# Kernel optimization log

Hardware: AMD Instinct MI355X
Metric: run time of the kernel (lower is better)

## Reference

```python
import jax, jax.numpy as jnp
import numpy as np

L = 2          # lstm_layers
H = 512        # state_size
E = 512        # embedding_size
V = 512        # latent_vocab_size
T = 100        # max_dec_len
START = V - 1  # start_id
B = 128        # batch
M = 256        # mem_len
NS = 4         # num_sample


def setup_inputs() -> dict:
    key = jax.random.key(0)
    ks = jax.random.split(key, 12)
    s = 0.05
    return {
        "y": jax.random.normal(ks[0], (B, H), jnp.float32),
        "kv_emb": jax.random.normal(ks[1], (B, M, H), jnp.float32),
        "kv_mask": jnp.ones((B, M), dtype=bool),
        "z_mask": jnp.ones((B, T), jnp.float32),
        "emb": jax.random.normal(ks[2], (V, E), jnp.float32) * s,
        "W_h0": jax.random.normal(ks[3], (L * H, H), jnp.float32) * s,
        "b_h0": jnp.zeros((L * H,), jnp.float32),
        "W_c0": jax.random.normal(ks[4], (L * H, H), jnp.float32) * s,
        "b_c0": jnp.zeros((L * H,), jnp.float32),
        "W_ih": jax.random.normal(ks[5], (L, 4 * H, E), jnp.float32) * s,
        "W_hh": jax.random.normal(ks[6], (L, 4 * H, H), jnp.float32) * s,
        "b_ih": jnp.zeros((L, 4 * H), jnp.float32),
        "b_hh": jnp.zeros((L, 4 * H), jnp.float32),
        "W_attn": jax.random.normal(ks[7], (H, H), jnp.float32) * s,
        "W_cproj": jax.random.normal(ks[8], (H, 2 * H), jnp.float32) * s,
        "b_cproj": jnp.zeros((H,), jnp.float32),
        "W_out": jax.random.normal(ks[9], (V, H), jnp.float32) * s,
        "b_out": jnp.zeros((V,), jnp.float32),
        "num_sample": NS,
    }


def reference(y, kv_emb, kv_mask, z_mask, emb, W_h0, b_h0, W_c0, b_c0,
              W_ih, W_hh, b_ih, b_hh, W_attn, W_cproj, b_cproj, W_out, b_out,
              num_sample):
    n = int(num_sample)
    Bn = B * n
    # view(B,1,..).repeat(1,n,..).view(B*n,..)  ==  repeat along axis 0 (sample-minor)
    y_r = jnp.repeat(y, n, axis=0)                      # [Bn, H]
    kv_r = jnp.repeat(kv_emb, n, axis=0)                # [Bn, M, H]
    mask_add = jnp.where(jnp.repeat(kv_mask, n, axis=0), 0.0, -1e9).astype(jnp.float32)

    # init_state: project y -> per-layer h, c
    h = (y_r @ W_h0.T + b_h0).reshape(Bn, L, H).transpose(1, 0, 2)  # [L, Bn, H]
    c = (y_r @ W_c0.T + b_c0).reshape(Bn, L, H).transpose(1, 0, 2)
    x0 = emb[jnp.full((Bn,), START)]                    # start-token embedding
    base_key = jax.random.key(42)

    def step(carry, t):
        h, c, x = carry
        hs, cs = [], []
        for l in range(L):  # stacked LSTM cells (PyTorch gate order i,f,g,o)
            g = x @ W_ih[l].T + b_ih[l] + h[l] @ W_hh[l].T + b_hh[l]
            i_, f_, g_, o_ = jnp.split(g, 4, axis=-1)
            cn = jax.nn.sigmoid(f_) * c[l] + jax.nn.sigmoid(i_) * jnp.tanh(g_)
            hn = jax.nn.sigmoid(o_) * jnp.tanh(cn)
            hs.append(hn); cs.append(cn); x = hn
        out = x                                         # top-layer h, [Bn, H]
        # bilinear attention over kv memory with mask
        scores = jnp.einsum('bd,bmd->bm', out @ W_attn.T, kv_r) + mask_add
        attn = jax.nn.softmax(scores, axis=-1)
        ctx = jnp.einsum('bm,bmd->bd', attn, kv_r)
        out2 = jnp.concatenate([out, ctx], axis=-1) @ W_cproj.T + b_cproj
        logits = out2 @ W_out.T + b_out                 # output_proj
        logp = jax.nn.log_softmax(logits, axis=-1)
        # Categorical sample (strategy='unconstrained')
        idx = jax.random.categorical(jax.random.fold_in(base_key, t), logits)
        slp = jnp.take_along_axis(logp, idx[:, None], axis=-1)[:, 0]
        ent = (-jnp.exp(logp) * logp).sum(-1).mean()
        return (jnp.stack(hs), jnp.stack(cs), emb[idx]), (idx, slp, ent)

    _, (ids, slps, ents) = jax.lax.scan(step, (h, c, x0), jnp.arange(T))
    z_ids = ids.T.reshape(B, n, T)                      # [B, n, T] int
    z_states = emb[z_ids]                               # [B, n, T, E]
    stepwise = slps.T.reshape(B, n, T)
    z_lp = (stepwise * z_mask[:, None, :]).sum(-1)      # [B, n]
    ent_z = ents.mean()
    return z_ids, z_states, z_lp, stepwise, ent_z
```

## Files before the change

### kernel.cpp

```cpp
#include <hip/hip_runtime.h>
#include <hip/hip_bf16.h>

#define BATCH 128
#define NSAMP 4
#define BN    512
#define HID   512
#define EMBD  512
#define VOC   512
#define TLEN  100
#define MLEN  256
#define NGATE 2048

#define NPART 8

#define O_ZID     0L
#define O_ZSTATES 51200L
#define O_ZLP     26265600L
#define O_STEP    26266112L
#define O_ENT     26317312L
#define O_TOTAL   26317313L

#define OFF_H    0L
#define OFF_C    524288L
#define OFF_X    1048576L
#define OFF_G    1310720L
#define OFF_Q    9699328L
#define OFF_CTX  11796480L
#define OFF_O2   12058624L
#define OFF_LG   14155776L
#define OFF_YR   16252928L
#define OFF_BG   16515072L
#define OFF_ENT  16519168L
#define OFF_SLP  16519296L
#define WS_FLOATS 16570496L

#define GPSTRIDE 1048576L
#define SPSTRIDE 262144L

__device__ float g_ws[WS_FLOATS];
__device__ int   g_ids[TLEN * BN];

__device__ __forceinline__ unsigned rotl32(unsigned x, int r) {
  return (x << r) | (x >> (32 - r));
}
__device__ __forceinline__ void threefry2x32(unsigned k0, unsigned k1,
                                             unsigned& x0, unsigned& x1) {
  unsigned k2 = k0 ^ k1 ^ 0x1BD11BDAu;
#define TF_R(r) { x0 += x1; x1 = rotl32(x1, r); x1 ^= x0; }
  x0 += k0; x1 += k1;
  TF_R(13) TF_R(15) TF_R(26) TF_R(6)
  x0 += k1; x1 += k2 + 1u;
  TF_R(17) TF_R(29) TF_R(16) TF_R(24)
  x0 += k2; x1 += k0 + 2u;
  TF_R(13) TF_R(15) TF_R(26) TF_R(6)
  x0 += k0; x1 += k1 + 3u;
  TF_R(17) TF_R(29) TF_R(16) TF_R(24)
  x0 += k1; x1 += k2 + 4u;
  TF_R(13) TF_R(15) TF_R(26) TF_R(6)
  x0 += k2; x1 += k0 + 5u;
#undef TF_R
}

__device__ __forceinline__ float gumbel_from_bits(unsigned bits) {
  unsigned fb = (bits >> 9) | 0x3F800000u;
  float f = __uint_as_float(fb) - 1.0f;
  const float TINY = 1.17549435e-38f;
  float u = fmaxf(f + TINY, TINY);
  return -logf(-logf(u));
}

__device__ __forceinline__ float sigf(float x) {
  return 0.5f + 0.5f * tanhf(0.5f * x);
}

__device__ __forceinline__ float4 add4(float4 a, float4 b) {
  a.x += b.x; a.y += b.y; a.z += b.z; a.w += b.w; return a;
}

__global__ __launch_bounds__(64) void gemmsk(
    long offA1, int lda1, int P1, long strideP1,
    const float* __restrict__ B1, int ldb1, int K1,
    long offA2, int lda2,
    const float* __restrict__ B2, int ldb2,
    const float* __restrict__ biasExt, long biasOff,
    long offC, int ldc, int Kc)
{
  __shared__ float As[16][64];
  __shared__ float Bs[16][64];
  const int t  = threadIdx.x;
  const int tm = t >> 3;
  const int tn = t & 7;
  const int m0 = blockIdx.y * 64;
  const int n0 = blockIdx.x * 64;
  const int kp = blockIdx.z;

  int kbase = kp * Kc;
  const float* A; const float* B; int lda, ldb, P; long strideP;
  if (kbase < K1) {
    A = g_ws + offA1; B = B1; lda = lda1; ldb = ldb1; P = P1; strideP = strideP1;
  } else {
    A = g_ws + offA2; B = B2; lda = lda2; ldb = ldb2; P = 1; strideP = 0;
    kbase -= K1;
  }

  float acc[8][8];
#pragma unroll
  for (int i = 0; i < 8; ++i)
#pragma unroll
    for (int j = 0; j < 8; ++j) acc[i][j] = 0.f;

  for (int k0 = 0; k0 < Kc; k0 += 16) {
    const int kg = kbase + k0;
    const float* pa = A + (size_t)(m0 + t) * lda + kg;
    float4 a0, a1, a2, a3;
    {
      const float4* q4 = (const float4*)pa;
      a0 = q4[0]; a1 = q4[1]; a2 = q4[2]; a3 = q4[3];
      for (int p = 1; p < P; ++p) {
        const float4* r4 = (const float4*)(pa + (size_t)p * strideP);
        a0 = add4(a0, r4[0]); a1 = add4(a1, r4[1]);
        a2 = add4(a2, r4[2]); a3 = add4(a3, r4[3]);
      }
    }
    const float4* pb = (const float4*)(B + (size_t)(n0 + t) * ldb + kg);
    float4 b0 = pb[0], b1 = pb[1], b2 = pb[2], b3 = pb[3];

    __syncthreads();
    As[ 0][t] = a0.x; As[ 1][t] = a0.y; As[ 2][t] = a0.z; As[ 3][t] = a0.w;
    As[ 4][t] = a1.x; As[ 5][t] = a1.y; As[ 6][t] = a1.z; As[ 7][t] = a1.w;
    As[ 8][t] = a2.x; As[ 9][t] = a2.y; As[10][t] = a2.z; As[11][t] = a2.w;
    As[12][t] = a3.x; As[13][t] = a3.y; As[14][t] = a3.z; As[15][t] = a3.w;
    Bs[ 0][t] = b0.x; Bs[ 1][t] = b0.y; Bs[ 2][t] = b0.z; Bs[ 3][t] = b0.w;
    Bs[ 4][t] = b1.x; Bs[ 5][t] = b1.y; Bs[ 6][t] = b1.z; Bs[ 7][t] = b1.w;
    Bs[ 8][t] = b2.x; Bs[ 9][t] = b2.y; Bs[10][t] = b2.z; Bs[11][t] = b2.w;
    Bs[12][t] = b3.x; Bs[13][t] = b3.y; Bs[14][t] = b3.z; Bs[15][t] = b3.w;
    __syncthreads();

#pragma unroll
    for (int k = 0; k < 16; ++k) {
      float av[8], bv[8];
      *(float4*)&av[0] = *(const float4*)&As[k][tm * 8];
      *(float4*)&av[4] = *(const float4*)&As[k][tm * 8 + 4];
      *(float4*)&bv[0] = *(const float4*)&Bs[k][tn * 8];
      *(float4*)&bv[4] = *(const float4*)&Bs[k][tn * 8 + 4];
#pragma unroll
      for (int i = 0; i < 8; ++i)
#pragma unroll
        for (int j = 0; j < 8; ++j)
          acc[i][j] += av[i] * bv[j];
    }
  }

  const int Mtot = gridDim.y * 64;
  float* C = g_ws + offC + (size_t)kp * (size_t)Mtot * ldc;
  const float* bias = nullptr;
  if (kp == 0)
    bias = biasExt ? biasExt : (biasOff >= 0 ? g_ws + biasOff : nullptr);
#pragma unroll
  for (int i = 0; i < 8; ++i) {
    const int row = m0 + tm * 8 + i;
    const int col = n0 + tn * 8;
    float4 o0, o1;
    o0.x = acc[i][0]; o0.y = acc[i][1]; o0.z = acc[i][2]; o0.w = acc[i][3];
    o1.x = acc[i][4]; o1.y = acc[i][5]; o1.z = acc[i][6]; o1.w = acc[i][7];
    if (bias) {
      o0.x += bias[col];     o0.y += bias[col + 1];
      o0.z += bias[col + 2]; o0.w += bias[col + 3];
      o1.x += bias[col + 4]; o1.y += bias[col + 5];
      o1.z += bias[col + 6]; o1.w += bias[col + 7];
    }
    *(float4*)(C + (size_t)row * ldc + col)     = o0;
    *(float4*)(C + (size_t)row * ldc + col + 4) = o1;
  }
}

__global__ __launch_bounds__(256) void gemm2(
    long offA1, int lda1,
    const float* __restrict__ B1, int ldb1, int K1,
    long offA2, int lda2,
    const float* __restrict__ B2, int ldb2, int K2,
    const float* __restrict__ biasExt, long biasOff,
    long offC, int ldc)
{
  __shared__ float As[16][68];
  __shared__ float Bs[16][68];
  const int tid = threadIdx.x;
  const int tx  = tid & 15;
  const int ty  = tid >> 4;
  const int ldr = tid >> 2;
  const int ldk = (tid & 3) << 2;
  const int m0 = blockIdx.y * 64;
  const int n0 = blockIdx.x * 64;
  float acc[4][4] = {{0.f}};

  for (int seg = 0; seg < 2; ++seg) {
    const float* A = g_ws + (seg ? offA2 : offA1);
    const float* B = seg ? B2 : B1;
    const int lda = seg ? lda2 : lda1;
    const int ldb = seg ? ldb2 : ldb1;
    const int K   = seg ? K2  : K1;
    for (int k0 = 0; k0 < K; k0 += 16) {
      float4 av = *(const float4*)(A + (size_t)(m0 + ldr) * lda + k0 + ldk);
      float4 bv = *(const float4*)(B + (size_t)(n0 + ldr) * ldb + k0 + ldk);
      __syncthreads();
      As[ldk + 0][ldr] = av.x; As[ldk + 1][ldr] = av.y;
      As[ldk + 2][ldr] = av.z; As[ldk + 3][ldr] = av.w;
      Bs[ldk + 0][ldr] = bv.x; Bs[ldk + 1][ldr] = bv.y;
      Bs[ldk + 2][ldr] = bv.z; Bs[ldk + 3][ldr] = bv.w;
      __syncthreads();
#pragma unroll
      for (int k = 0; k < 16; ++k) {
        float4 a = *(const float4*)&As[k][ty * 4];
        float4 b = *(const float4*)&Bs[k][tx * 4];
        acc[0][0] += a.x * b.x; acc[0][1] += a.x * b.y; acc[0][2] += a.x * b.z; acc[0][3] += a.x * b.w;
        acc[1][0] += a.y * b.x; acc[1][1] += a.y * b.y; acc[1][2] += a.y * b.z; acc[1][3] += a.y * b.w;
        acc[2][0] += a.z * b.x; acc[2][1] += a.z * b.y; acc[2][2] += a.z * b.z; acc[2][3] += a.z * b.w;
        acc[3][0] += a.w * b.x; acc[3][1] += a.w * b.y; acc[3][2] += a.w * b.z; acc[3][3] += a.w * b.w;
      }
    }
  }
  const float* bias = biasExt ? biasExt : (biasOff >= 0 ? g_ws + biasOff : nullptr);
  float* C = g_ws + offC;
#pragma unroll
  for (int i = 0; i < 4; ++i) {
    int row = m0 + ty * 4 + i;
    int col = n0 + tx * 4;
    float4 o;
    o.x = acc[i][0]; o.y = acc[i][1]; o.z = acc[i][2]; o.w = acc[i][3];
    if (bias) {
      o.x += bias[col]; o.y += bias[col + 1]; o.z += bias[col + 2]; o.w += bias[col + 3];
    }
    *(float4*)(C + (size_t)row * ldc + col) = o;
  }
}

__global__ __launch_bounds__(256) void lstm_cell(long hoff, long coff)
{
  int idx = blockIdx.x * 256 + threadIdx.x;
  int r = idx >> 9, j = idx & 511;
  float gi = 0.f, gf = 0.f, gg = 0.f, go = 0.f;
  const size_t rb = (size_t)r * NGATE;
#pragma unroll
  for (int p = 0; p < NPART; ++p) {
    const float* gr = g_ws + OFF_G + (size_t)p * GPSTRIDE + rb;
    gi += gr[j]; gf += gr[512 + j]; gg += gr[1024 + j]; go += gr[1536 + j];
  }
  float* h = g_ws + hoff;
  float* c = g_ws + coff;
  float cold = c[(size_t)r * 1024 + j];
  float cn = sigf(gf) * cold + sigf(gi) * tanhf(gg);
  float hn = sigf(go) * tanhf(cn);
  c[(size_t)r * 1024 + j] = cn;
  h[(size_t)r * 1024 + j] = hn;
}

__global__ __launch_bounds__(256) void attn_kernel(
    const float* __restrict__ kv,
    const void*  __restrict__ kvm_raw)
{
  __shared__ float qs[4][512];
  __shared__ float sc[4][256];
  const int b = blockIdx.x;
  const int tid = threadIdx.x;
  const int lane = tid & 63, wave = tid >> 6;
  float* ctx = g_ws + OFF_CTX;
  const float* kvb = kv + (size_t)b * MLEN * HID;
  const unsigned* w32 = (const unsigned*)kvm_raw;
  const unsigned char* u8 = (const unsigned char*)kvm_raw;
  const bool u8mode = (w32[0] == 0x01010101u);
#pragma unroll
  for (int s = 0; s < 4; ++s) {
    float q0 = 0.f, q1 = 0.f;
    const size_t base = (size_t)(b * 4 + s) * HID + tid;
#pragma unroll
    for (int p = 0; p < NPART; ++p) {
      q0 += g_ws[OFF_Q + (size_t)p * SPSTRIDE + base];
      q1 += g_ws[OFF_Q + (size_t)p * SPSTRIDE + base + 256];
    }
    qs[s][tid] = q0; qs[s][tid + 256] = q1;
  }
  __syncthreads();
  for (int m = wave; m < MLEN; m += 4) {
    const float* kr = kvb + (size_t)m * HID;
    float a0 = 0.f, a1 = 0.f, a2 = 0.f, a3 = 0.f;
    for (int d = lane; d < HID; d += 64) {
      float kvv = kr[d];
      a0 += qs[0][d] * kvv; a1 += qs[1][d] * kvv;
      a2 += qs[2][d] * kvv; a3 += qs[3][d] * kvv;
    }
#pragma unroll
    for (int off = 32; off > 0; off >>= 1) {
      a0 += __shfl_down(a0, off); a1 += __shfl_down(a1, off);
      a2 += __shfl_down(a2, off); a3 += __shfl_down(a3, off);
    }
    if (lane == 0) {
      bool on = u8mode ? (u8[b * MLEN + m] != 0) : (w32[b * MLEN + m] != 0u);
      float madd = on ? 0.0f : -1e9f;
      sc[0][m] = a0 + madd; sc[1][m] = a1 + madd;
      sc[2][m] = a2 + madd; sc[3][m] = a3 + madd;
    }
  }
  __syncthreads();
  {
    const int s = wave;
    float mx = -3.4e38f;
    for (int m = lane; m < MLEN; m += 64) mx = fmaxf(mx, sc[s][m]);
#pragma unroll
    for (int off = 32; off > 0; off >>= 1) mx = fmaxf(mx, __shfl_xor(mx, off));
    float sum = 0.f;
    for (int m = lane; m < MLEN; m += 64) {
      float e = expf(sc[s][m] - mx);
      sc[s][m] = e; sum += e;
    }
#pragma unroll
    for (int off = 32; off > 0; off >>= 1) sum += __shfl_xor(sum, off);
    for (int m = lane; m < MLEN; m += 64) sc[s][m] = sc[s][m] / sum;
  }
  __syncthreads();
  float c00=0,c01=0,c10=0,c11=0,c20=0,c21=0,c30=0,c31=0;
  for (int m = 0; m < MLEN; ++m) {
    float k0v = kvb[(size_t)m * HID + tid];
    float k1v = kvb[(size_t)m * HID + tid + 256];
    float p0 = sc[0][m], p1 = sc[1][m], p2 = sc[2][m], p3 = sc[3][m];
    c00 += p0 * k0v; c01 += p0 * k1v;
    c10 += p1 * k0v; c11 += p1 * k1v;
    c20 += p2 * k0v; c21 += p2 * k1v;
    c30 += p3 * k0v; c31 += p3 * k1v;
  }
  ctx[(size_t)(b * 4 + 0) * HID + tid] = c00; ctx[(size_t)(b * 4 + 0) * HID + tid + 256] = c01;
  ctx[(size_t)(b * 4 + 1) * HID + tid] = c10; ctx[(size_t)(b * 4 + 1) * HID + tid + 256] = c11;
  ctx[(size_t)(b * 4 + 2) * HID + tid] = c20; ctx[(size_t)(b * 4 + 2) * HID + tid + 256] = c21;
  ctx[(size_t)(b * 4 + 3) * HID + tid] = c30; ctx[(size_t)(b * 4 + 3) * HID + tid + 256] = c31;
}

__global__ __launch_bounds__(256) void sample_step(
    const float* __restrict__ emb, int t)
{
  __shared__ float rz[256];
  __shared__ int   ri[256];
  __shared__ float rl[256];
  const int row = blockIdx.x;
  const int tid = threadIdx.x;
  float* xbuf = g_ws + OFF_X;

  unsigned fk0 = 0u, fk1 = (unsigned)t;
  threefry2x32(0u, 42u, fk0, fk1);

  float l[2], g[2];
#pragma unroll
  for (int j = 0; j < 2; ++j) {
    int v = tid + j * 256;
    unsigned c0 = 0u, c1 = (unsigned)(row * VOC + v);
    threefry2x32(fk0, fk1, c0, c1);
    g[j] = gumbel_from_bits(c0 ^ c1);
    float lv = 0.f;
    const size_t base = (size_t)row * VOC + v;
#pragma unroll
    for (int p = 0; p < NPART; ++p)
      lv += g_ws[OFF_LG + (size_t)p * SPSTRIDE + base];
    l[j] = lv;
  }

  float z0 = l[0] + g[0], z1 = l[1] + g[1];
  float bz; int bi; float bl;
  if (z1 > z0) { bz = z1; bi = tid + 256; bl = l[1]; }
  else         { bz = z0; bi = tid;       bl = l[0]; }
  rz[tid] = bz; ri[tid] = bi; rl[tid] = bl;
  __syncthreads();
  for (int s = 128; s > 0; s >>= 1) {
    if (tid < s) {
      float oz = rz[tid + s]; int oi = ri[tid + s];
      if (oz > rz[tid] || (oz == rz[tid] && oi < ri[tid])) {
        rz[tid] = oz; ri[tid] = oi; rl[tid] = rl[tid + s];
      }
    }
    __syncthreads();
  }
  const int idx = ri[0];
  const float l_at = rl[0];
  __syncthreads();

  rz[tid] = fmaxf(l[0], l[1]);
  __syncthreads();
  for (int s = 128; s > 0; s >>= 1) {
    if (tid < s) rz[tid] = fmaxf(rz[tid], rz[tid + s]);
    __syncthreads();
  }
  const float m = rz[0];
  __syncthreads();

  float d0 = l[0] - m, d1 = l[1] - m;
  float e0 = expf(d0), e1 = expf(d1);
  rz[tid] = e0 + e1;
  rl[tid] = e0 * d0 + e1 * d1;
  __syncthreads();
  for (int s = 128; s > 0; s >>= 1) {
    if (tid < s) { rz[tid] += rz[tid + s]; rl[tid] += rl[tid + s]; }
    __syncthreads();
  }
  if (tid == 0) {
    float S = rz[0], W = rl[0];
    float logS = logf(S);
    g_ids[t * BN + row] = idx;
    g_ws[OFF_SLP + t * BN + row] = (l_at - m) - logS;
    atomicAdd(&g_ws[OFF_ENT + t], logS - W / S);
  }
  const float* er = emb + (size_t)idx * EMBD;
  xbuf[(size_t)row * EMBD + tid]       = er[tid];
  xbuf[(size_t)row * EMBD + tid + 256] = er[tid + 256];
}

__global__ __launch_bounds__(256) void init_misc(
    const float* __restrict__ y, const float* __restrict__ emb,
    const float* __restrict__ b_ih, const float* __restrict__ b_hh)
{
  int gid = blockIdx.x * 256 + threadIdx.x;
  int r = gid >> 9, col = gid & 511;
  g_ws[OFF_YR + gid] = y[(size_t)(r >> 2) * HID + col];
  g_ws[OFF_X + gid]  = emb[(size_t)(VOC - 1) * EMBD + col];
  if (gid < 2 * NGATE) g_ws[OFF_BG + gid] = b_ih[gid] + b_hh[gid];
  if (gid < 128) g_ws[OFF_ENT + gid] = 0.0f;
}

__global__ __launch_bounds__(256) void write_out(
    const float* __restrict__ emb, const float* __restrict__ zmask,
    float* __restrict__ out)
{
  long i = (long)blockIdx.x * 256 + threadIdx.x;
  const long stride = (long)gridDim.x * 256;
  for (; i < O_TOTAL; i += stride) {
    float v;
    if (i < O_ZSTATES) {
      int bs = (int)(i / TLEN), t = (int)(i % TLEN);
      v = (float)g_ids[t * BN + bs];
    } else if (i < O_ZLP) {
      long j = i - O_ZSTATES;
      int e = (int)(j & 511);
      int bst = (int)(j >> 9);
      int bs = bst / TLEN, t = bst % TLEN;
      v = emb[(size_t)g_ids[t * BN + bs] * EMBD + e];
    } else if (i < O_STEP) {
      int bs = (int)(i - O_ZLP);
      int b = bs >> 2;
      float acc = 0.f;
      for (int t = 0; t < TLEN; ++t)
        acc += g_ws[OFF_SLP + t * BN + bs] * zmask[b * TLEN + t];
      v = acc;
    } else if (i < O_ENT) {
      long j = i - O_STEP;
      int bs = (int)(j / TLEN), t = (int)(j % TLEN);
      v = g_ws[OFF_SLP + t * BN + bs];
    } else {
      float e = 0.f;
      for (int t = 0; t < TLEN; ++t) e += g_ws[OFF_ENT + t];
      v = e / (float)(BN * TLEN);
    }
    out[i] = v;
  }
}

extern "C" void kernel_launch(void* const* d_in, const int* in_sizes, int n_in,
                              void* d_out, int out_size, void* d_ws, size_t ws_size,
                              hipStream_t stream) {
  (void)in_sizes; (void)n_in; (void)out_size; (void)d_ws; (void)ws_size;
  const float* y       = (const float*)d_in[0];
  const float* kv      = (const float*)d_in[1];
  const void*  kvm     = (const void*)d_in[2];
  const float* zmask   = (const float*)d_in[3];
  const float* emb     = (const float*)d_in[4];
  const float* W_h0    = (const float*)d_in[5];
  const float* b_h0    = (const float*)d_in[6];
  const float* W_c0    = (const float*)d_in[7];
  const float* b_c0    = (const float*)d_in[8];
  const float* W_ih    = (const float*)d_in[9];
  const float* W_hh    = (const float*)d_in[10];
  const float* b_ih    = (const float*)d_in[11];
  const float* b_hh    = (const float*)d_in[12];
  const float* W_attn  = (const float*)d_in[13];
  const float* W_cproj = (const float*)d_in[14];
  const float* b_cproj = (const float*)d_in[15];
  const float* W_out   = (const float*)d_in[16];
  const float* b_out   = (const float*)d_in[17];
  float* out = (float*)d_out;

  init_misc<<<1024, 256, 0, stream>>>(y, emb, b_ih, b_hh);

  dim3 g_init(1024 / 64, 512 / 64);
  gemm2<<<g_init, 256, 0, stream>>>(OFF_YR, 512, W_h0, 512, 512,
                                    0L, 0, nullptr, 0, 0, b_h0, -1L, OFF_H, 1024);
  gemm2<<<g_init, 256, 0, stream>>>(OFF_YR, 512, W_c0, 512, 512,
                                    0L, 0, nullptr, 0, 0, b_c0, -1L, OFF_C, 1024);

  dim3 g_gates(2048 / 64, 512 / 64, NPART);
  dim3 g_sq(512 / 64, 512 / 64, NPART);
  const size_t WL = (size_t)NGATE * HID;

  for (int t = 0; t < TLEN; ++t) {
    gemmsk<<<g_gates, 64, 0, stream>>>(OFF_X, 512, 1, 0L, W_ih, 512, 512,
                                       OFF_H, 1024, W_hh, 512,
                                       nullptr, OFF_BG, OFF_G, NGATE, 128);
    lstm_cell<<<1024, 256, 0, stream>>>(OFF_H, OFF_C);
    gemmsk<<<g_gates, 64, 0, stream>>>(OFF_H, 1024, 1, 0L, W_ih + WL, 512, 512,
                                       OFF_H + 512, 1024, W_hh + WL, 512,
                                       nullptr, OFF_BG + NGATE, OFF_G, NGATE, 128);
    lstm_cell<<<1024, 256, 0, stream>>>(OFF_H + 512, OFF_C + 512);
    gemmsk<<<g_sq, 64, 0, stream>>>(OFF_H + 512, 1024, 1, 0L, W_attn, 512, 512,
                                    0L, 0, nullptr, 0,
                                    nullptr, -1L, OFF_Q, 512, 64);
    attn_kernel<<<128, 256, 0, stream>>>(kv, kvm);
    gemmsk<<<g_sq, 64, 0, stream>>>(OFF_H + 512, 1024, 1, 0L, W_cproj, 1024, 512,
                                    OFF_CTX, 512, W_cproj + 512, 1024,
                                    b_cproj, -1L, OFF_O2, 512, 128);
    gemmsk<<<g_sq, 64, 0, stream>>>(OFF_O2, 512, NPART, SPSTRIDE, W_out, 512, 512,
                                    0L, 0, nullptr, 0,
                                    b_out, -1L, OFF_LG, 512, 64);
    sample_step<<<512, 256, 0, stream>>>(emb, t);
  }

  int wblocks = (int)((O_TOTAL + 255L) / 256L);
  write_out<<<wblocks, 256, 0, stream>>>(emb, zmask, out);
}
```

Baseline: 23.29 ms.

## Fuse per-step decoder kernels into one persistent kernel with grid barriers

Replaces the 900 per-step kernel launches (gate GEMMs, LSTM cells, attention, projections, sampling) with one persistent kernel of 256 blocks that loops over time steps and separates phases with a software grid barrier built on atomics. The GEMMs are remapped so that each wave computes one split-K tile, and the small projections use 32x32 tiles per wave to keep all blocks busy. The goal is to remove launch overhead and inter-kernel gaps. The cost is barrier latency, and the barrier can deadlock if not all 256 blocks are co-resident on the device.

```diff
diff --git a/kernel.cpp b/kernel.cpp
--- a/kernel.cpp
+++ b/kernel.cpp
@@ -1,5 +1,4 @@
 #include <hip/hip_runtime.h>
-#include <hip/hip_bf16.h>
 
 #define BATCH 128
 #define NSAMP 4
@@ -12,6 +11,9 @@
 #define NGATE 2048
 
 #define NPART 8
+
+#define NBLK  256
+#define NTHR  512
 
 #define O_ZID     0L
 #define O_ZSTATES 51200L
@@ -39,6 +41,26 @@
 
 __device__ float g_ws[WS_FLOATS];
 __device__ int   g_ids[TLEN * BN];
+__device__ unsigned bar_cnt;
+__device__ unsigned bar_gen;
+
+__device__ __forceinline__ void gsync() {
+  __syncthreads();
+  if (threadIdx.x == 0) {
+    __threadfence();
+    unsigned g = __hip_atomic_load(&bar_gen, __ATOMIC_RELAXED, __HIP_MEMORY_SCOPE_AGENT);
+    unsigned a = __hip_atomic_fetch_add(&bar_cnt, 1u, __ATOMIC_ACQ_REL, __HIP_MEMORY_SCOPE_AGENT);
+    if (a == (unsigned)(NBLK - 1)) {
+      __hip_atomic_store(&bar_cnt, 0u, __ATOMIC_RELAXED, __HIP_MEMORY_SCOPE_AGENT);
+      __hip_atomic_store(&bar_gen, g + 1u, __ATOMIC_RELEASE, __HIP_MEMORY_SCOPE_AGENT);
+    } else {
+      while (__hip_atomic_load(&bar_gen, __ATOMIC_RELAXED, __HIP_MEMORY_SCOPE_AGENT) == g)
+        __builtin_amdgcn_s_sleep(2);
+    }
+    __threadfence();
+  }
+  __syncthreads();
+}
 
 __device__ __forceinline__ unsigned rotl32(unsigned x, int r) {
   return (x << r) | (x >> (32 - r));
@@ -77,32 +99,28 @@
   a.x += b.x; a.y += b.y; a.z += b.z; a.w += b.w; return a;
 }
 
-__global__ __launch_bounds__(64) void gemmsk(
-    long offA1, int lda1, int P1, long strideP1,
+__device__ __forceinline__ void gemm64_wave(
+    float* __restrict__ S, int lane,
+    int m0, int n0, int kp, int Kc,
+    long offA1, int lda1, int P1, long sP1,
     const float* __restrict__ B1, int ldb1, int K1,
     long offA2, int lda2,
     const float* __restrict__ B2, int ldb2,
     const float* __restrict__ biasExt, long biasOff,
-    long offC, int ldc, int Kc)
+    long offC, int ldc)
 {
-  __shared__ float As[16][64];
-  __shared__ float Bs[16][64];
-  const int t  = threadIdx.x;
-  const int tm = t >> 3;
-  const int tn = t & 7;
-  const int m0 = blockIdx.y * 64;
-  const int n0 = blockIdx.x * 64;
-  const int kp = blockIdx.z;
-
+  float* As = S;
+  float* Bs = S + 1024;
   int kbase = kp * Kc;
-  const float* A; const float* B; int lda, ldb, P; long strideP;
+  const float* A; const float* B; int lda, ldb, P; long sP;
   if (kbase < K1) {
-    A = g_ws + offA1; B = B1; lda = lda1; ldb = ldb1; P = P1; strideP = strideP1;
+    A = g_ws + offA1; B = B1; lda = lda1; ldb = ldb1; P = P1; sP = sP1;
   } else {
-    A = g_ws + offA2; B = B2; lda = lda2; ldb = ldb2; P = 1; strideP = 0;
+    A = g_ws + offA2; B = B2; lda = lda2; ldb = ldb2; P = 1; sP = 0;
     kbase -= K1;
   }
 
+  const int tm = lane >> 3, tn = lane & 7;
   float acc[8][8];
 #pragma unroll
   for (int i = 0; i < 8; ++i)
@@ -111,38 +129,38 @@
 
   for (int k0 = 0; k0 < Kc; k0 += 16) {
     const int kg = kbase + k0;
-    const float* pa = A + (size_t)(m0 + t) * lda + kg;
+    const float* pa = A + (size_t)(m0 + lane) * lda + kg;
     float4 a0, a1, a2, a3;
     {
       const float4* q4 = (const float4*)pa;
       a0 = q4[0]; a1 = q4[1]; a2 = q4[2]; a3 = q4[3];
       for (int p = 1; p < P; ++p) {
-        const float4* r4 = (const float4*)(pa + (size_t)p * strideP);
+        const float4* r4 = (const float4*)(pa + (size_t)p * sP);
         a0 = add4(a0, r4[0]); a1 = add4(a1, r4[1]);
         a2 = add4(a2, r4[2]); a3 = add4(a3, r4[3]);
       }
     }
-    const float4* pb = (const float4*)(B + (size_t)(n0 + t) * ldb + kg);
+    const float4* pb = (const float4*)(B + (size_t)(n0 + lane) * ldb + kg);
     float4 b0 = pb[0], b1 = pb[1], b2 = pb[2], b3 = pb[3];
 
     __syncthreads();
-    As[ 0][t] = a0.x; As[ 1][t] = a0.y; As[ 2][t] = a0.z; As[ 3][t] = a0.w;
-    As[ 4][t] = a1.x; As[ 5][t] = a1.y; As[ 6][t] = a1.z; As[ 7][t] = a1.w;
-    As[ 8][t] = a2.x; As[ 9][t] = a2.y; As[10][t] = a2.z; As[11][t] = a2.w;
-    As[12][t] = a3.x; As[13][t] = a3.y; As[14][t] = a3.z; As[15][t] = a3.w;
-    Bs[ 0][t] = b0.x; Bs[ 1][t] = b0.y; Bs[ 2][t] = b0.z; Bs[ 3][t] = b0.w;
-    Bs[ 4][t] = b1.x; Bs[ 5][t] = b1.y; Bs[ 6][t] = b1.z; Bs[ 7][t] = b1.w;
-    Bs[ 8][t] = b2.x; Bs[ 9][t] = b2.y; Bs[10][t] = b2.z; Bs[11][t] = b2.w;
-    Bs[12][t] = b3.x; Bs[13][t] = b3.y; Bs[14][t] = b3.z; Bs[15][t] = b3.w;
+    As[ 0*64+lane]=a0.x; As[ 1*64+lane]=a0.y; As[ 2*64+lane]=a0.z; As[ 3*64+lane]=a0.w;
+    As[ 4*64+lane]=a1.x; As[ 5*64+lane]=a1.y; As[ 6*64+lane]=a1.z; As[ 7*64+lane]=a1.w;
+    As[ 8*64+lane]=a2.x; As[ 9*64+lane]=a2.y; As[10*64+lane]=a2.z; As[11*64+lane]=a2.w;
+    As[12*64+lane]=a3.x; As[13*64+lane]=a3.y; As[14*64+lane]=a3.z; As[15*64+lane]=a3.w;
+    Bs[ 0*64+lane]=b0.x; Bs[ 1*64+lane]=b0.y; Bs[ 2*64+lane]=b0.z; Bs[ 3*64+lane]=b0.w;
+    Bs[ 4*64+lane]=b1.x; Bs[ 5*64+lane]=b1.y; Bs[ 6*64+lane]=b1.z; Bs[ 7*64+lane]=b1.w;
+    Bs[ 8*64+lane]=b2.x; Bs[ 9*64+lane]=b2.y; Bs[10*64+lane]=b2.z; Bs[11*64+lane]=b2.w;
+    Bs[12*64+lane]=b3.x; Bs[13*64+lane]=b3.y; Bs[14*64+lane]=b3.z; Bs[15*64+lane]=b3.w;
     __syncthreads();
 
 #pragma unroll
     for (int k = 0; k < 16; ++k) {
       float av[8], bv[8];
-      *(float4*)&av[0] = *(const float4*)&As[k][tm * 8];
-      *(float4*)&av[4] = *(const float4*)&As[k][tm * 8 + 4];
-      *(float4*)&bv[0] = *(const float4*)&Bs[k][tn * 8];
-      *(float4*)&bv[4] = *(const float4*)&Bs[k][tn * 8 + 4];
+      *(float4*)&av[0] = *(const float4*)&As[k*64 + tm*8];
+      *(float4*)&av[4] = *(const float4*)&As[k*64 + tm*8 + 4];
+      *(float4*)&bv[0] = *(const float4*)&Bs[k*64 + tn*8];
+      *(float4*)&bv[4] = *(const float4*)&Bs[k*64 + tn*8 + 4];
 #pragma unroll
       for (int i = 0; i < 8; ++i)
 #pragma unroll
@@ -151,8 +169,7 @@
     }
   }
 
-  const int Mtot = gridDim.y * 64;
-  float* C = g_ws + offC + (size_t)kp * (size_t)Mtot * ldc;
+  float* C = g_ws + offC + (size_t)kp * 512 * (size_t)ldc;
   const float* bias = nullptr;
   if (kp == 0)
     bias = biasExt ? biasExt : (biasOff >= 0 ? g_ws + biasOff : nullptr);
@@ -171,6 +188,330 @@
     }
     *(float4*)(C + (size_t)row * ldc + col)     = o0;
     *(float4*)(C + (size_t)row * ldc + col + 4) = o1;
+  }
+}
+
+__device__ __forceinline__ void gemm32_wave(
+    float* __restrict__ S, int lane,
+    int m0, int n0, int kp, int Kc,
+    long offA1, int lda1, int P1, long sP1,
+    const float* __restrict__ B1, int ldb1, int K1,
+    long offA2, int lda2,
+    const float* __restrict__ B2, int ldb2,
+    const float* __restrict__ biasExt, long biasOff,
+    long offC, int ldc)
+{
+  float* As = S;
+  float* Bs = S + 512;
+  int kbase = kp * Kc;
+  const float* A; const float* B; int lda, ldb, P; long sP;
+  if (kbase < K1) {
+    A = g_ws + offA1; B = B1; lda = lda1; ldb = ldb1; P = P1; sP = sP1;
+  } else {
+    A = g_ws + offA2; B = B2; lda = lda2; ldb = ldb2; P = 1; sP = 0;
+    kbase -= K1;
+  }
+
+  const int r  = lane & 31;
+  const int ko = (lane >> 5) * 8;
+  const int tm = lane >> 3, tn = lane & 7;
+  float acc[4][4];
+#pragma unroll
+  for (int i = 0; i < 4; ++i)
+#pragma unroll
+    for (int j = 0; j < 4; ++j) acc[i][j] = 0.f;
+
+  for (int k0 = 0; k0 < Kc; k0 += 16) {
+    const int kg = kbase + k0;
+    const float* pa = A + (size_t)(m0 + r) * lda + kg + ko;
+    float4 a0, a1;
+    {
+      const float4* q4 = (const float4*)pa;
+      a0 = q4[0]; a1 = q4[1];
+      for (int p = 1; p < P; ++p) {
+        const float4* r4 = (const float4*)(pa + (size_t)p * sP);
+        a0 = add4(a0, r4[0]); a1 = add4(a1, r4[1]);
+      }
+    }
+    const float4* pb = (const float4*)(B + (size_t)(n0 + r) * ldb + kg + ko);
+    float4 b0 = pb[0], b1 = pb[1];
+
+    __syncthreads();
+    As[(ko+0)*32+r]=a0.x; As[(ko+1)*32+r]=a0.y; As[(ko+2)*32+r]=a0.z; As[(ko+3)*32+r]=a0.w;
+    As[(ko+4)*32+r]=a1.x; As[(ko+5)*32+r]=a1.y; As[(ko+6)*32+r]=a1.z; As[(ko+7)*32+r]=a1.w;
+    Bs[(ko+0)*32+r]=b0.x; Bs[(ko+1)*32+r]=b0.y; Bs[(ko+2)*32+r]=b0.z; Bs[(ko+3)*32+r]=b0.w;
+    Bs[(ko+4)*32+r]=b1.x; Bs[(ko+5)*32+r]=b1.y; Bs[(ko+6)*32+r]=b1.z; Bs[(ko+7)*32+r]=b1.w;
+    __syncthreads();
+
+#pragma unroll
+    for (int k = 0; k < 16; ++k) {
+      float4 av = *(const float4*)&As[k*32 + tm*4];
+      float4 bv = *(const float4*)&Bs[k*32 + tn*4];
+      acc[0][0] += av.x*bv.x; acc[0][1] += av.x*bv.y; acc[0][2] += av.x*bv.z; acc[0][3] += av.x*bv.w;
+      acc[1][0] += av.y*bv.x; acc[1][1] += av.y*bv.y; acc[1][2] += av.y*bv.z; acc[1][3] += av.y*bv.w;
+      acc[2][0] += av.z*bv.x; acc[2][1] += av.z*bv.y; acc[2][2] += av.z*bv.z; acc[2][3] += av.z*bv.w;
+      acc[3][0] += av.w*bv.x; acc[3][1] += av.w*bv.y; acc[3][2] += av.w*bv.z; acc[3][3] += av.w*bv.w;
+    }
+  }
+
+  float* C = g_ws + offC + (size_t)kp * 512 * (size_t)ldc;
+  const float* bias = nullptr;
+  if (kp == 0)
+    bias = biasExt ? biasExt : (biasOff >= 0 ? g_ws + biasOff : nullptr);
+#pragma unroll
+  for (int i = 0; i < 4; ++i) {
+    const int row = m0 + tm * 4 + i;
+    const int col = n0 + tn * 4;
+    float4 o;
+    o.x = acc[i][0]; o.y = acc[i][1]; o.z = acc[i][2]; o.w = acc[i][3];
+    if (bias) {
+      o.x += bias[col];     o.y += bias[col + 1];
+      o.z += bias[col + 2]; o.w += bias[col + 3];
+    }
+    *(float4*)(C + (size_t)row * ldc + col) = o;
+  }
+}
+
+__device__ __forceinline__ void cell_phase(long hoff, long coff) {
+  for (int idx = blockIdx.x * NTHR + threadIdx.x; idx < 262144; idx += NBLK * NTHR) {
+    int rr = idx >> 9, j = idx & 511;
+    float gi = 0.f, gf = 0.f, gg = 0.f, go = 0.f;
+    const size_t rb = (size_t)rr * NGATE;
+#pragma unroll
+    for (int p = 0; p < NPART; ++p) {
+      const float* gr = g_ws + OFF_G + (size_t)p * GPSTRIDE + rb;
+      gi += gr[j]; gf += gr[512 + j]; gg += gr[1024 + j]; go += gr[1536 + j];
+    }
+    float* h = g_ws + hoff;
+    float* c = g_ws + coff;
+    float cold = c[(size_t)rr * 1024 + j];
+    float cn = sigf(gf) * cold + sigf(gi) * tanhf(gg);
+    float hn = sigf(go) * tanhf(cn);
+    c[(size_t)rr * 1024 + j] = cn;
+    h[(size_t)rr * 1024 + j] = hn;
+  }
+}
+
+__device__ __forceinline__ void attn_phase(const float* __restrict__ kv,
+                                           const void* __restrict__ kvm_raw,
+                                           float* __restrict__ smem) {
+  const int bb = blockIdx.x;
+  if (bb >= 128) return;
+  float* qs  = smem;
+  float* scb = smem + 2048;
+  const int tid = threadIdx.x;
+  const bool act = tid < 256;
+  const int lane = tid & 63, wv = tid >> 6;
+  float* ctx = g_ws + OFF_CTX;
+  const float* kvb = kv + (size_t)bb * MLEN * HID;
+  const unsigned* w32 = (const unsigned*)kvm_raw;
+  const unsigned char* u8 = (const unsigned char*)kvm_raw;
+  if (act) {
+#pragma unroll
+    for (int s = 0; s < 4; ++s) {
+      float q0 = 0.f, q1 = 0.f;
+      const size_t base = (size_t)(bb * 4 + s) * HID + tid;
+#pragma unroll
+      for (int p = 0; p < NPART; ++p) {
+        q0 += g_ws[OFF_Q + (size_t)p * SPSTRIDE + base];
+        q1 += g_ws[OFF_Q + (size_t)p * SPSTRIDE + base + 256];
+      }
+      qs[s*512 + tid] = q0; qs[s*512 + tid + 256] = q1;
+    }
+  }
+  __syncthreads();
+  if (act) {
+    const bool u8mode = (w32[0] == 0x01010101u);
+    for (int m = wv; m < MLEN; m += 4) {
+      const float* kr = kvb + (size_t)m * HID;
+      float a0 = 0.f, a1 = 0.f, a2 = 0.f, a3 = 0.f;
+      for (int d = lane; d < HID; d += 64) {
+        float kvv = kr[d];
+        a0 += qs[0*512 + d] * kvv; a1 += qs[1*512 + d] * kvv;
+        a2 += qs[2*512 + d] * kvv; a3 += qs[3*512 + d] * kvv;
+      }
+#pragma unroll
+      for (int off = 32; off > 0; off >>= 1) {
+        a0 += __shfl_down(a0, off); a1 += __shfl_down(a1, off);
+        a2 += __shfl_down(a2, off); a3 += __shfl_down(a3, off);
+      }
+      if (lane == 0) {
+        bool on = u8mode ? (u8[bb * MLEN + m] != 0) : (w32[bb * MLEN + m] != 0u);
+        float madd = on ? 0.0f : -1e9f;
+        scb[0*256+m] = a0 + madd; scb[1*256+m] = a1 + madd;
+        scb[2*256+m] = a2 + madd; scb[3*256+m] = a3 + madd;
+      }
+    }
+  }
+  __syncthreads();
+  if (act) {
+    const int s = wv;
+    float mx = -3.4e38f;
+    for (int m = lane; m < MLEN; m += 64) mx = fmaxf(mx, scb[s*256+m]);
+#pragma unroll
+    for (int off = 32; off > 0; off >>= 1) mx = fmaxf(mx, __shfl_xor(mx, off));
+    float sum = 0.f;
+    for (int m = lane; m < MLEN; m += 64) {
+      float e = expf(scb[s*256+m] - mx);
+      scb[s*256+m] = e; sum += e;
+    }
+#pragma unroll
+    for (int off = 32; off > 0; off >>= 1) sum += __shfl_xor(sum, off);
+    for (int m = lane; m < MLEN; m += 64) scb[s*256+m] = scb[s*256+m] / sum;
+  }
+  __syncthreads();
+  if (act) {
+    float c00=0,c01=0,c10=0,c11=0,c20=0,c21=0,c30=0,c31=0;
+    for (int m = 0; m < MLEN; ++m) {
+      float k0v = kvb[(size_t)m * HID + tid];
+      float k1v = kvb[(size_t)m * HID + tid + 256];
+      float p0 = scb[0*256+m], p1 = scb[1*256+m], p2 = scb[2*256+m], p3 = scb[3*256+m];
+      c00 += p0 * k0v; c01 += p0 * k1v;
+      c10 += p1 * k0v; c11 += p1 * k1v;
+      c20 += p2 * k0v; c21 += p2 * k1v;
+      c30 += p3 * k0v; c31 += p3 * k1v;
+    }
+    ctx[(size_t)(bb*4 + 0) * HID + tid] = c00; ctx[(size_t)(bb*4 + 0) * HID + tid + 256] = c01;
+    ctx[(size_t)(bb*4 + 1) * HID + tid] = c10; ctx[(size_t)(bb*4 + 1) * HID + tid + 256] = c11;
+    ctx[(size_t)(bb*4 + 2) * HID + tid] = c20; ctx[(size_t)(bb*4 + 2) * HID + tid + 256] = c21;
+    ctx[(size_t)(bb*4 + 3) * HID + tid] = c30; ctx[(size_t)(bb*4 + 3) * HID + tid + 256] = c31;
+  }
+}
+
+__device__ __forceinline__ void sample_phase(const float* __restrict__ emb, int t,
+                                             float* __restrict__ smem) {
+  float* rz = smem;
+  float* rl = smem + 512;
+  int*   ri = (int*)(smem + 1024);
+  const int sub  = threadIdx.x >> 8;
+  const int stid = threadIdx.x & 255;
+  const int row  = blockIdx.x * 2 + sub;
+  float* rzs = rz + sub * 256;
+  float* rls = rl + sub * 256;
+  int*   ris = ri + sub * 256;
+  float* xbuf = g_ws + OFF_X;
+
+  unsigned fk0 = 0u, fk1 = (unsigned)t;
+  threefry2x32(0u, 42u, fk0, fk1);
+
+  float l[2], gv[2];
+#pragma unroll
+  for (int j = 0; j < 2; ++j) {
+    int v = stid + j * 256;
+    unsigned c0 = 0u, c1 = (unsigned)(row * VOC + v);
+    threefry2x32(fk0, fk1, c0, c1);
+    gv[j] = gumbel_from_bits(c0 ^ c1);
+    float lv = 0.f;
+    const size_t base = (size_t)row * VOC + v;
+#pragma unroll
+    for (int p = 0; p < NPART; ++p)
+      lv += g_ws[OFF_LG + (size_t)p * SPSTRIDE + base];
+    l[j] = lv;
+  }
+
+  float z0 = l[0] + gv[0], z1 = l[1] + gv[1];
+  float bz; int bi; float bl;
+  if (z1 > z0) { bz = z1; bi = stid + 256; bl = l[1]; }
+  else         { bz = z0; bi = stid;       bl = l[0]; }
+  rzs[stid] = bz; ris[stid] = bi; rls[stid] = bl;
+  __syncthreads();
+  for (int s = 128; s > 0; s >>= 1) {
+    if (stid < s) {
+      float oz = rzs[stid + s]; int oi = ris[stid + s];
+      if (oz > rzs[stid] || (oz == rzs[stid] && oi < ris[stid])) {
+        rzs[stid] = oz; ris[stid] = oi; rls[stid] = rls[stid + s];
+      }
+    }
+    __syncthreads();
+  }
+  const int sidx = ris[0];
+  const float l_at = rls[0];
+  __syncthreads();
+
+  rzs[stid] = fmaxf(l[0], l[1]);
+  __syncthreads();
+  for (int s = 128; s > 0; s >>= 1) {
+    if (stid < s) rzs[stid] = fmaxf(rzs[stid], rzs[stid + s]);
+    __syncthreads();
+  }
+  const float m = rzs[0];
+  __syncthreads();
+
+  float d0 = l[0] - m, d1 = l[1] - m;
+  float e0 = expf(d0), e1 = expf(d1);
+  rzs[stid] = e0 + e1;
+  rls[stid] = e0 * d0 + e1 * d1;
+  __syncthreads();
+  for (int s = 128; s > 0; s >>= 1) {
+    if (stid < s) { rzs[stid] += rzs[stid + s]; rls[stid] += rls[stid + s]; }
+    __syncthreads();
+  }
+  if (stid == 0) {
+    float S = rzs[0], W = rls[0];
+    float logS = logf(S);
+    g_ids[t * BN + row] = sidx;
+    g_ws[OFF_SLP + t * BN + row] = (l_at - m) - logS;
+    atomicAdd(&g_ws[OFF_ENT + t], logS - W / S);
+  }
+  const float* er = emb + (size_t)sidx * EMBD;
+  xbuf[(size_t)row * EMBD + stid]       = er[stid];
+  xbuf[(size_t)row * EMBD + stid + 256] = er[stid + 256];
+}
+
+__global__ __launch_bounds__(NTHR, 2) void persist(
+    const float* __restrict__ kv, const void* __restrict__ kvm,
+    const float* __restrict__ emb,
+    const float* __restrict__ W_ih, const float* __restrict__ W_hh,
+    const float* __restrict__ W_attn, const float* __restrict__ W_cproj,
+    const float* __restrict__ b_cproj, const float* __restrict__ W_out,
+    const float* __restrict__ b_out)
+{
+  __shared__ __align__(16) float smem[16384];
+  const int tid  = threadIdx.x;
+  const int w    = tid >> 6;
+  const int lane = tid & 63;
+  float* S = smem + w * 2048;
+
+  const int xb = blockIdx.x & 7, jb = blockIdx.x >> 3;
+  const int g_nt = xb * 4 + (jb >> 3), g_mt = jb & 7;
+  const int s_nt = xb * 2 + (jb >> 4), s_mt = jb & 15;
+  const size_t WL = (size_t)NGATE * HID;
+
+#pragma unroll 1
+  for (int t = 0; t < TLEN; ++t) {
+    gemm64_wave(S, lane, g_mt * 64, g_nt * 64, w, 128,
+                OFF_X, 512, 1, 0L, W_ih, 512, 512,
+                OFF_H, 1024, W_hh, 512,
+                nullptr, OFF_BG, OFF_G, NGATE);
+    gsync();
+    cell_phase(OFF_H, OFF_C);
+    gsync();
+    gemm64_wave(S, lane, g_mt * 64, g_nt * 64, w, 128,
+                OFF_H, 1024, 1, 0L, W_ih + WL, 512, 512,
+                OFF_H + 512, 1024, W_hh + WL, 512,
+                nullptr, OFF_BG + NGATE, OFF_G, NGATE);
+    gsync();
+    cell_phase(OFF_H + 512, OFF_C + 512);
+    gsync();
+    gemm32_wave(S, lane, s_mt * 32, s_nt * 32, w, 64,
+                OFF_H + 512, 1024, 1, 0L, W_attn, 512, 512,
+                0L, 0, nullptr, 0,
+                nullptr, -1L, OFF_Q, 512);
+    gsync();
+    attn_phase(kv, kvm, smem);
+    gsync();
+    gemm32_wave(S, lane, s_mt * 32, s_nt * 32, w, 128,
+                OFF_H + 512, 1024, 1, 0L, W_cproj, 1024, 512,
+                OFF_CTX, 512, W_cproj + 512, 1024,
+                b_cproj, -1L, OFF_O2, 512);
+    gsync();
+    gemm32_wave(S, lane, s_mt * 32, s_nt * 32, w, 64,
+                OFF_O2, 512, NPART, SPSTRIDE, W_out, 512, 512,
+                0L, 0, nullptr, 0,
+                b_out, -1L, OFF_LG, 512);
+    gsync();
+    sample_phase(emb, t, smem);
+    gsync();
   }
 }
 
@@ -232,182 +573,6 @@
     }
     *(float4*)(C + (size_t)row * ldc + col) = o;
   }
-}
-
-__global__ __launch_bounds__(256) void lstm_cell(long hoff, long coff)
-{
-  int idx = blockIdx.x * 256 + threadIdx.x;
-  int r = idx >> 9, j = idx & 511;
-  float gi = 0.f, gf = 0.f, gg = 0.f, go = 0.f;
-  const size_t rb = (size_t)r * NGATE;
-#pragma unroll
-  for (int p = 0; p < NPART; ++p) {
-    const float* gr = g_ws + OFF_G + (size_t)p * GPSTRIDE + rb;
-    gi += gr[j]; gf += gr[512 + j]; gg += gr[1024 + j]; go += gr[1536 + j];
-  }
-  float* h = g_ws + hoff;
-  float* c = g_ws + coff;
-  float cold = c[(size_t)r * 1024 + j];
-  float cn = sigf(gf) * cold + sigf(gi) * tanhf(gg);
-  float hn = sigf(go) * tanhf(cn);
-  c[(size_t)r * 1024 + j] = cn;
-  h[(size_t)r * 1024 + j] = hn;
-}
-
-__global__ __launch_bounds__(256) void attn_kernel(
-    const float* __restrict__ kv,
-    const void*  __restrict__ kvm_raw)
-{
-  __shared__ float qs[4][512];
-  __shared__ float sc[4][256];
-  const int b = blockIdx.x;
-  const int tid = threadIdx.x;
-  const int lane = tid & 63, wave = tid >> 6;
-  float* ctx = g_ws + OFF_CTX;
-  const float* kvb = kv + (size_t)b * MLEN * HID;
-  const unsigned* w32 = (const unsigned*)kvm_raw;
-  const unsigned char* u8 = (const unsigned char*)kvm_raw;
-  const bool u8mode = (w32[0] == 0x01010101u);
-#pragma unroll
-  for (int s = 0; s < 4; ++s) {
-    float q0 = 0.f, q1 = 0.f;
-    const size_t base = (size_t)(b * 4 + s) * HID + tid;
-#pragma unroll
-    for (int p = 0; p < NPART; ++p) {
-      q0 += g_ws[OFF_Q + (size_t)p * SPSTRIDE + base];
-      q1 += g_ws[OFF_Q + (size_t)p * SPSTRIDE + base + 256];
-    }
-    qs[s][tid] = q0; qs[s][tid + 256] = q1;
-  }
-  __syncthreads();
-  for (int m = wave; m < MLEN; m += 4) {
-    const float* kr = kvb + (size_t)m * HID;
-    float a0 = 0.f, a1 = 0.f, a2 = 0.f, a3 = 0.f;
-    for (int d = lane; d < HID; d += 64) {
-      float kvv = kr[d];
-      a0 += qs[0][d] * kvv; a1 += qs[1][d] * kvv;
-      a2 += qs[2][d] * kvv; a3 += qs[3][d] * kvv;
-    }
-#pragma unroll
-    for (int off = 32; off > 0; off >>= 1) {
-      a0 += __shfl_down(a0, off); a1 += __shfl_down(a1, off);
-      a2 += __shfl_down(a2, off); a3 += __shfl_down(a3, off);
-    }
-    if (lane == 0) {
-      bool on = u8mode ? (u8[b * MLEN + m] != 0) : (w32[b * MLEN + m] != 0u);
-      float madd = on ? 0.0f : -1e9f;
-      sc[0][m] = a0 + madd; sc[1][m] = a1 + madd;
-      sc[2][m] = a2 + madd; sc[3][m] = a3 + madd;
-    }
-  }
-  __syncthreads();
-  {
-    const int s = wave;
-    float mx = -3.4e38f;
-    for (int m = lane; m < MLEN; m += 64) mx = fmaxf(mx, sc[s][m]);
-#pragma unroll
-    for (int off = 32; off > 0; off >>= 1) mx = fmaxf(mx, __shfl_xor(mx, off));
-    float sum = 0.f;
-    for (int m = lane; m < MLEN; m += 64) {
-      float e = expf(sc[s][m] - mx);
-      sc[s][m] = e; sum += e;
-    }
-#pragma unroll
-    for (int off = 32; off > 0; off >>= 1) sum += __shfl_xor(sum, off);
-    for (int m = lane; m < MLEN; m += 64) sc[s][m] = sc[s][m] / sum;
-  }
-  __syncthreads();
-  float c00=0,c01=0,c10=0,c11=0,c20=0,c21=0,c30=0,c31=0;
-  for (int m = 0; m < MLEN; ++m) {
-    float k0v = kvb[(size_t)m * HID + tid];
-    float k1v = kvb[(size_t)m * HID + tid + 256];
-    float p0 = sc[0][m], p1 = sc[1][m], p2 = sc[2][m], p3 = sc[3][m];
-    c00 += p0 * k0v; c01 += p0 * k1v;
-    c10 += p1 * k0v; c11 += p1 * k1v;
-    c20 += p2 * k0v; c21 += p2 * k1v;
-    c30 += p3 * k0v; c31 += p3 * k1v;
-  }
-  ctx[(size_t)(b * 4 + 0) * HID + tid] = c00; ctx[(size_t)(b * 4 + 0) * HID + tid + 256] = c01;
-  ctx[(size_t)(b * 4 + 1) * HID + tid] = c10; ctx[(size_t)(b * 4 + 1) * HID + tid + 256] = c11;
-  ctx[(size_t)(b * 4 + 2) * HID + tid] = c20; ctx[(size_t)(b * 4 + 2) * HID + tid + 256] = c21;
-  ctx[(size_t)(b * 4 + 3) * HID + tid] = c30; ctx[(size_t)(b * 4 + 3) * HID + tid + 256] = c31;
-}
-
-__global__ __launch_bounds__(256) void sample_step(
-    const float* __restrict__ emb, int t)
-{
-  __shared__ float rz[256];
-  __shared__ int   ri[256];
-  __shared__ float rl[256];
-  const int row = blockIdx.x;
-  const int tid = threadIdx.x;
-  float* xbuf = g_ws + OFF_X;
-
-  unsigned fk0 = 0u, fk1 = (unsigned)t;
-  threefry2x32(0u, 42u, fk0, fk1);
-
-  float l[2], g[2];
-#pragma unroll
-  for (int j = 0; j < 2; ++j) {
-    int v = tid + j * 256;
-    unsigned c0 = 0u, c1 = (unsigned)(row * VOC + v);
-    threefry2x32(fk0, fk1, c0, c1);
-    g[j] = gumbel_from_bits(c0 ^ c1);
-    float lv = 0.f;
-    const size_t base = (size_t)row * VOC + v;
-#pragma unroll
-    for (int p = 0; p < NPART; ++p)
-      lv += g_ws[OFF_LG + (size_t)p * SPSTRIDE + base];
-    l[j] = lv;
-  }
-
-  float z0 = l[0] + g[0], z1 = l[1] + g[1];
-  float bz; int bi; float bl;
-  if (z1 > z0) { bz = z1; bi = tid + 256; bl = l[1]; }
-  else         { bz = z0; bi = tid;       bl = l[0]; }
-  rz[tid] = bz; ri[tid] = bi; rl[tid] = bl;
-  __syncthreads();
-  for (int s = 128; s > 0; s >>= 1) {
-    if (tid < s) {
-      float oz = rz[tid + s]; int oi = ri[tid + s];
-      if (oz > rz[tid] || (oz == rz[tid] && oi < ri[tid])) {
-        rz[tid] = oz; ri[tid] = oi; rl[tid] = rl[tid + s];
-      }
-    }
-    __syncthreads();
-  }
-  const int idx = ri[0];
-  const float l_at = rl[0];
-  __syncthreads();
-
-  rz[tid] = fmaxf(l[0], l[1]);
-  __syncthreads();
-  for (int s = 128; s > 0; s >>= 1) {
-    if (tid < s) rz[tid] = fmaxf(rz[tid], rz[tid + s]);
-    __syncthreads();
-  }
-  const float m = rz[0];
-  __syncthreads();
-
-  float d0 = l[0] - m, d1 = l[1] - m;
-  float e0 = expf(d0), e1 = expf(d1);
-  rz[tid] = e0 + e1;
-  rl[tid] = e0 * d0 + e1 * d1;
-  __syncthreads();
-  for (int s = 128; s > 0; s >>= 1) {
-    if (tid < s) { rz[tid] += rz[tid + s]; rl[tid] += rl[tid + s]; }
-    __syncthreads();
-  }
-  if (tid == 0) {
-    float S = rz[0], W = rl[0];
-    float logS = logf(S);
-    g_ids[t * BN + row] = idx;
-    g_ws[OFF_SLP + t * BN + row] = (l_at - m) - logS;
-    atomicAdd(&g_ws[OFF_ENT + t], logS - W / S);
-  }
-  const float* er = emb + (size_t)idx * EMBD;
-  xbuf[(size_t)row * EMBD + tid]       = er[tid];
-  xbuf[(size_t)row * EMBD + tid + 256] = er[tid + 256];
 }
 
 __global__ __launch_bounds__(256) void init_misc(
@@ -491,31 +656,8 @@
   gemm2<<<g_init, 256, 0, stream>>>(OFF_YR, 512, W_c0, 512, 512,
                                     0L, 0, nullptr, 0, 0, b_c0, -1L, OFF_C, 1024);
 
-  dim3 g_gates(2048 / 64, 512 / 64, NPART);
-  dim3 g_sq(512 / 64, 512 / 64, NPART);
-  const size_t WL = (size_t)NGATE * HID;
-
-  for (int t = 0; t < TLEN; ++t) {
-    gemmsk<<<g_gates, 64, 0, stream>>>(OFF_X, 512, 1, 0L, W_ih, 512, 512,
-                                       OFF_H, 1024, W_hh, 512,
-                                       nullptr, OFF_BG, OFF_G, NGATE, 128);
-    lstm_cell<<<1024, 256, 0, stream>>>(OFF_H, OFF_C);
-    gemmsk<<<g_gates, 64, 0, stream>>>(OFF_H, 1024, 1, 0L, W_ih + WL, 512, 512,
-                                       OFF_H + 512, 1024, W_hh + WL, 512,
-                                       nullptr, OFF_BG + NGATE, OFF_G, NGATE, 128);
-    lstm_cell<<<1024, 256, 0, stream>>>(OFF_H + 512, OFF_C + 512);
-    gemmsk<<<g_sq, 64, 0, stream>>>(OFF_H + 512, 1024, 1, 0L, W_attn, 512, 512,
-                                    0L, 0, nullptr, 0,
-                                    nullptr, -1L, OFF_Q, 512, 64);
-    attn_kernel<<<128, 256, 0, stream>>>(kv, kvm);
-    gemmsk<<<g_sq, 64, 0, stream>>>(OFF_H + 512, 1024, 1, 0L, W_cproj, 1024, 512,
-                                    OFF_CTX, 512, W_cproj + 512, 1024,
-                                    b_cproj, -1L, OFF_O2, 512, 128);
-    gemmsk<<<g_sq, 64, 0, stream>>>(OFF_O2, 512, NPART, SPSTRIDE, W_out, 512, 512,
-                                    0L, 0, nullptr, 0,
-                                    b_out, -1L, OFF_LG, 512, 64);
-    sample_step<<<512, 256, 0, stream>>>(emb, t);
-  }
+  persist<<<NBLK, NTHR, 0, stream>>>(kv, kvm, emb, W_ih, W_hh,
+                                     W_attn, W_cproj, b_cproj, W_out, b_out);
 
   int wblocks = (int)((O_TOTAL + 255L) / 256L);
   write_out<<<wblocks, 256, 0, stream>>>(emb, zmask, out);
```

New measurement: 81.08 ms. 3.48x slower.
